# Kernel optimization log

Measured on AMD Instinct MI355X. Metric: run time of the kernel, lower is better.

## Reference

```python
import jax, jax.numpy as jnp
import numpy as np


def _adj(p):
    # p: [B,N,C] -> W = exp(-pairwise squared distance), fully dense (incl. self loops)
    sq = jnp.sum(p * p, axis=-1, keepdims=True)            # [B,N,1]
    d = sq - 2.0 * jnp.einsum('bnc,bmc->bnm', p, p) + jnp.swapaxes(sq, 1, 2)
    return jnp.exp(-d)


def _cheb_lap(W):
    # PyG ChebConv norm with sym normalization, lambda_max=2: L_hat = L - I = -D^{-1/2} W D^{-1/2}
    dinv = jax.lax.rsqrt(jnp.sum(W, axis=-1))              # [B,N]
    return -(dinv[:, :, None] * W * dinv[:, None, :])


def _reg_lap(W):
    # get_laplacian(sym) after remove_self_loops: L = I - D'^{-1/2} W' D'^{-1/2}, W' = W with zero diag
    N = W.shape[1]
    eye = jnp.eye(N, dtype=W.dtype)
    W0 = W * (1.0 - eye)
    dinv = jax.lax.rsqrt(jnp.sum(W0, axis=-1))
    return eye - dinv[:, :, None] * W0 * dinv[:, None, :]


def _cheb(x, Lhat, Wk, b):
    # Chebyshev recursion: Z0=x, Z1=L_hat x, Zk = 2 L_hat Z_{k-1} - Z_{k-2}
    # x: [B,N,Cin], Lhat: [B,N,N], Wk: [K,Cin,Cout]
    Z0 = x
    out = jnp.einsum('bni,io->bno', Z0, Wk[0])
    if Wk.shape[0] > 1:
        Z1 = jnp.einsum('bnm,bmi->bni', Lhat, x)
        out = out + jnp.einsum('bni,io->bno', Z1, Wk[1])
        for k in range(2, Wk.shape[0]):
            Z2 = 2.0 * jnp.einsum('bnm,bmi->bni', Lhat, Z1) - Z0
            out = out + jnp.einsum('bni,io->bno', Z2, Wk[k])
            Z0, Z1 = Z1, Z2
    return out + b


def _reg(out, L):
    # ||out^T L out||_F, block-diagonal L -> sum over batch blocks
    M = jnp.einsum('bnc,bnm,bmd->cd', out, L, out)
    return jnp.linalg.norm(M)


def setup_inputs() -> dict:
    key = jax.random.key(0)
    ks = jax.random.split(key, 16)
    B, N = 16, 1024
    s = 0.05
    return {
        'x': jax.random.normal(ks[0], (B, N, 6), dtype=jnp.float32),
        'batch': jnp.repeat(jnp.arange(B, dtype=jnp.int64 if jax.config.jax_enable_x64 else jnp.int32), N),
        'batch_size': B,
        'nr_points': N,
        'w1': jax.random.normal(ks[1], (6, 6, 128), dtype=jnp.float32) * s,
        'b1': jnp.zeros((128,), dtype=jnp.float32),
        'w2': jax.random.normal(ks[2], (5, 128, 512), dtype=jnp.float32) * s,
        'b2': jnp.zeros((512,), dtype=jnp.float32),
        'w3': jax.random.normal(ks[3], (3, 512, 1024), dtype=jnp.float32) * s,
        'b3': jnp.zeros((1024,), dtype=jnp.float32),
        'fw1': jax.random.normal(ks[4], (1024, 512), dtype=jnp.float32) * s,
        'fb1': jnp.zeros((512,), dtype=jnp.float32),
        'fw2': jax.random.normal(ks[5], (512, 128), dtype=jnp.float32) * s,
        'fb2': jnp.zeros((128,), dtype=jnp.float32),
        'fw3': jax.random.normal(ks[6], (128, 10), dtype=jnp.float32) * s,
        'fb3': jnp.zeros((10,), dtype=jnp.float32),
    }


def reference(x, batch, batch_size, nr_points, w1, b1, w2, b2, w3, b3,
              fw1, fb1, fw2, fb2, fw3, fb3):
    sg = jax.lax.stop_gradient
    # reshape of x happens inside torch.no_grad -> input to conv1 is detached
    h = sg(x)
    W1 = sg(_adj(x))
    out = jax.nn.relu(_cheb(h, _cheb_lap(W1), w1, b1))            # [B,N,128]
    r1 = sg(_reg(out, _reg_lap(W1)))
    W2 = sg(_adj(out))
    out = jax.nn.relu(_cheb(out, sg(_cheb_lap(W2)), w2, b2))      # [B,N,512]
    r2 = sg(_reg(out, _reg_lap(W2)))
    W3 = sg(_adj(out))
    out = jax.nn.relu(_cheb(out, sg(_cheb_lap(W3)), w3, b3))      # [B,N,1024]
    r3 = sg(_reg(out, _reg_lap(W3)))
    pooled = jnp.max(out, axis=1)                                  # MaxPool1d over points
    h = jax.nn.relu(pooled @ fw1 + fb1)
    h = jax.nn.relu(h @ fw2 + fb2)
    logits = h @ fw3 + fb3
    return logits, r1, r2, r3
```

## Files before the change

kernel.cpp:

```cpp
#include <hip/hip_runtime.h>

#define BB 16
#define NN 1024
#define LDT 16384

typedef float4 f4;
typedef __attribute__((ext_vector_type(8))) short bf16x8;
typedef __attribute__((ext_vector_type(4))) float f32x4;

__device__ __forceinline__ unsigned f2b1(float f) {
    unsigned u = __builtin_bit_cast(unsigned, f);
    return (u + 0x7fffu + ((u >> 16) & 1u)) >> 16;
}
__device__ __forceinline__ float b2f1(unsigned s) {
    unsigned u = (s & 0xffffu) << 16;
    return __builtin_bit_cast(float, u);
}

#define SW(r, k) ((r) * 64 + ((k) ^ (((((r) & 7) ^ (((r) >> 3) & 7))) << 3)))

__device__ __forceinline__ void gload16(const unsigned short* g, short* l) {
    __builtin_amdgcn_global_load_lds(
        (const __attribute__((address_space(1))) unsigned int*)g,
        (__attribute__((address_space(3))) unsigned int*)l, 16, 0, 0);
}

__device__ __forceinline__ float wave_sum(float v) {
    #pragma unroll
    for (int m = 32; m >= 1; m >>= 1) v += __shfl_xor(v, m);
    return v;
}
__device__ __forceinline__ float wave_max(float v) {
    #pragma unroll
    for (int m = 32; m >= 1; m >>= 1) v = fmaxf(v, __shfl_xor(v, m));
    return v;
}

__device__ __forceinline__ void stage_tr(short* T, const unsigned short* src,
                                         size_t col_base, int c0, int Cvalid, int tid) {
    #pragma unroll
    for (int n = 0; n < 2; n++) {
        int q = n * 256 + tid;
        int p = q >> 4, h = q & 15;
        int cg = c0 + 2 * p;
        uint4 r0 = make_uint4(0, 0, 0, 0), r1 = make_uint4(0, 0, 0, 0);
        if (cg < Cvalid)     r0 = *(const uint4*)&src[(size_t)cg * LDT + col_base + 8 * h];
        if (cg + 1 < Cvalid) r1 = *(const uint4*)&src[(size_t)(cg + 1) * LDT + col_base + 8 * h];
        const unsigned* a0 = (const unsigned*)&r0;
        const unsigned* a1 = (const unsigned*)&r1;
        #pragma unroll
        for (int e = 0; e < 8; e++) {
            unsigned lo = (e & 1) ? (a0[e >> 1] >> 16) : (a0[e >> 1] & 0xffffu);
            unsigned hi = (e & 1) ? (a1[e >> 1] >> 16) : (a1[e >> 1] & 0xffffu);
            int r = 8 * h + e;
            *(unsigned*)&T[SW(r, 2 * p)] = lo | (hi << 16);
        }
    }
}

__global__ void xt_prep_kernel(const float* __restrict__ x, short* __restrict__ xh,
                               short* __restrict__ xl) {
    int m = blockIdx.x * 256 + threadIdx.x;
    #pragma unroll
    for (int c = 0; c < 8; c++) {
        float v = (c < 6) ? x[(size_t)m * 6 + c] : 0.f;
        unsigned h = f2b1(v);
        unsigned l = f2b1(v - b2f1(h));
        xh[(size_t)c * LDT + m] = (short)h;
        xl[(size_t)c * LDT + m] = (short)l;
    }
}

__global__ void wtt_prep_kernel(const float* __restrict__ Wk, short* __restrict__ WtT,
                                int Kp64, int KpValid, int CpadM1, int shift, int Cin, int Cout) {
    int idx = blockIdx.x * 256 + threadIdx.x;
    if (idx >= Cout * Kp64) return;
    int co = idx / Kp64, kk = idx - co * Kp64;
    int c = kk & CpadM1;
    float val = 0.f;
    if (kk < KpValid && c < Cin)
        val = Wk[((size_t)(kk >> shift) * Cin + c) * Cout + co];
    WtT[(size_t)co * Kp64 + kk] = (short)f2b1(val);
}

__global__ void wtrans_kernel(const float* __restrict__ Wt, float* __restrict__ WtT,
                              int K, int O) {
    int idx = blockIdx.x * 256 + threadIdx.x;
    if (idx >= K * O) return;
    int o = idx / K, k = idx - o * K;
    WtT[idx] = Wt[(size_t)k * O + o];
}

__global__ void scale_sc_kernel(const short* __restrict__ src, const float* __restrict__ coeff,
                                short* __restrict__ dst, int total8) {
    int q = blockIdx.x * 256 + threadIdx.x;
    if (q >= total8) return;
    size_t base = (size_t)q * 8;
    int m8 = (int)(base & (LDT - 1));
    uint4 v = *(const uint4*)&((const unsigned short*)src)[base];
    f4 c0 = *(const f4*)&coeff[m8];
    f4 c1 = *(const f4*)&coeff[m8 + 4];
    const float* cp0 = (const float*)&c0;
    const float* cp1 = (const float*)&c1;
    unsigned* vp = (unsigned*)&v;
    #pragma unroll
    for (int e = 0; e < 4; e++) {
        float se0 = (e < 2) ? cp0[2 * e] : cp1[2 * e - 4];
        float se1 = (e < 2) ? cp0[2 * e + 1] : cp1[2 * e - 3];
        vp[e] = f2b1(b2f1(vp[e]) * se0) | (f2b1(b2f1(vp[e] >> 16) * se1) << 16);
    }
    *(uint4*)&((unsigned short*)dst)[base] = v;
}

__global__ __launch_bounds__(256)
void xpose_kernel(const short* __restrict__ H, const short* __restrict__ L,
                  int Cvalid, int CR, short* __restrict__ XRh, short* __restrict__ XRl) {
    __shared__ short Th[128 * 64], Tl[128 * 64];
    int tid = threadIdx.x;
    int m0 = blockIdx.x * 128, c0 = blockIdx.y * 64;
    stage_tr(Th, (const unsigned short*)H, m0, c0, Cvalid, tid);
    stage_tr(Tl, (const unsigned short*)L, m0, c0, Cvalid, tid);
    __syncthreads();
    #pragma unroll
    for (int n = 0; n < 4; n++) {
        int q = n * 256 + tid;
        int r = q >> 3, j = q & 7;
        int g = (r & 7) ^ ((r >> 3) & 7);
        *(uint4*)&XRh[(size_t)(m0 + r) * CR + c0 + 8 * j] = *(const uint4*)&Th[r * 64 + 8 * (j ^ g)];
        *(uint4*)&XRl[(size_t)(m0 + r) * CR + c0 + 8 * j] = *(const uint4*)&Tl[r * 64 + 8 * (j ^ g)];
    }
}

__global__ void sqt_part_kernel(const short* __restrict__ H, const short* __restrict__ L,
                                int C, float* __restrict__ dst) {
    int m = blockIdx.x * 256 + threadIdx.x;
    int cb = blockIdx.y * 128;
    int ce = min(cb + 128, C);
    const unsigned short* Hp = (const unsigned short*)H;
    const unsigned short* Lp = (const unsigned short*)L;
    float s = 0.f;
    for (int c = cb; c < ce; c++) {
        float v = b2f1(Hp[(size_t)c * LDT + m]) + b2f1(Lp[(size_t)c * LDT + m]);
        s += v * v;
    }
    dst[(size_t)blockIdx.y * LDT + m] = s;
}
__global__ void sqt_red_kernel(const float* __restrict__ part, int NC, float* __restrict__ sq) {
    int m = blockIdx.x * 256 + threadIdx.x;
    float s = 0.f;
    for (int y = 0; y < NC; y++) s += part[(size_t)y * LDT + m];
    sq[m] = s;
}

__global__ __launch_bounds__(256)
void adj_mfma_kernel(const short* __restrict__ XRh, const short* __restrict__ XRl,
                     int ck64, int CR, const float* __restrict__ sq,
                     short* __restrict__ Wb, float* __restrict__ Wpart,
                     float* __restrict__ diagW) {
    __shared__ short Ah[128 * 64], Al[128 * 64], Bh[128 * 64], Bl[128 * 64];
    __shared__ float jpart[128][2];
    int tid = threadIdx.x, lane = tid & 63, w = tid >> 6;
    int wj = w >> 1, wi = w & 1;
    int b = blockIdx.z, i0 = blockIdx.x * 128, j0 = blockIdx.y * 128;
    size_t bo = (size_t)b * NN;
    f32x4 acc[4][4] = {};
    const unsigned short* Hp = (const unsigned short*)XRh;
    const unsigned short* Lp = (const unsigned short*)XRl;
    int rr = lane >> 3, jj = lane & 7;
    size_t offI[4], offJ[4];
    #pragma unroll
    for (int m = 0; m < 4; m++) {
        int s = w + m * 4;
        int jc = jj ^ rr ^ (s & 7);
        offI[m] = (size_t)(bo + i0 + 8 * s + rr) * CR + 8 * jc;
        offJ[m] = (size_t)(bo + j0 + 8 * s + rr) * CR + 8 * jc;
    }
    for (int t = 0; t < ck64; t++) {
        int c0 = t * 64;
        #pragma unroll
        for (int m = 0; m < 4; m++) {
            int s512 = (w + m * 4) * 512;
            gload16(Hp + offI[m] + c0, Ah + s512);
            gload16(Lp + offI[m] + c0, Al + s512);
            gload16(Hp + offJ[m] + c0, Bh + s512);
            gload16(Lp + offJ[m] + c0, Bl + s512);
        }
        __syncthreads();
        int la = lane & 15;
        #pragma unroll
        for (int ks = 0; ks < 2; ks++) {
            int kb = ks * 32 + (lane >> 4) * 8;
            bf16x8 jh[4], jl[4], ih[4], il[4];
            #pragma unroll
            for (int f = 0; f < 4; f++) {
                int jr = wj * 64 + f * 16 + la;
                jh[f] = *(const bf16x8*)&Bh[SW(jr, kb)];
                jl[f] = *(const bf16x8*)&Bl[SW(jr, kb)];
                int ir = wi * 64 + f * 16 + la;
                ih[f] = *(const bf16x8*)&Ah[SW(ir, kb)];
                il[f] = *(const bf16x8*)&Al[SW(ir, kb)];
            }
            #pragma unroll
            for (int fq = 0; fq < 4; fq++)
                #pragma unroll
                for (int fi = 0; fi < 4; fi++) {
                    acc[fq][fi] = __builtin_amdgcn_mfma_f32_16x16x32_bf16(jh[fq], ih[fi], acc[fq][fi], 0, 0, 0);
                    acc[fq][fi] = __builtin_amdgcn_mfma_f32_16x16x32_bf16(jh[fq], il[fi], acc[fq][fi], 0, 0, 0);
                    acc[fq][fi] = __builtin_amdgcn_mfma_f32_16x16x32_bf16(jl[fq], ih[fi], acc[fq][fi], 0, 0, 0);
                }
        }
        __syncthreads();
    }
    const float* sqb = sq + bo;
    unsigned short* Wout = (unsigned short*)Wb + bo * NN;
    float si_[4];
    int iloc[4];
    #pragma unroll
    for (int fi = 0; fi < 4; fi++) {
        iloc[fi] = i0 + wi * 64 + fi * 16 + (lane & 15);
        si_[fi] = sqb[iloc[fi]];
    }
    #pragma unroll
    for (int fq = 0; fq < 4; fq++) {
        int jb = j0 + wj * 64 + fq * 16 + (lane >> 4) * 4;
        #pragma unroll
        for (int r = 0; r < 4; r++) {
            int j = jb + r;
            float sj = sqb[j];
            float p = 0.f;
            #pragma unroll
            for (int fi = 0; fi < 4; fi++) {
                float val = __expf(2.f * ((const float*)&acc[fq][fi])[r] - si_[fi] - sj);
                Wout[(size_t)j * NN + iloc[fi]] = (unsigned short)f2b1(val);
                if (iloc[fi] == j) diagW[bo + j] = val;
                else p += val;
            }
            p += __shfl_xor(p, 1); p += __shfl_xor(p, 2);
            p += __shfl_xor(p, 4); p += __shfl_xor(p, 8);
            if ((lane & 15) == 0)
                jpart[wj * 64 + fq * 16 + (lane >> 4) * 4 + r][wi] = p;
        }
    }
    __syncthreads();
    if (tid < 128)
        Wpart[(size_t)blockIdx.x * (BB * NN) + bo + j0 + tid] = jpart[tid][0] + jpart[tid][1];
}

__global__ void reduce_prep_kernel(const float* __restrict__ Wpart, const float* __restrict__ diagW,
                                   float* dinv, float* dinvP, float* cA1, float* cA2, float* cAV) {
    int idx = blockIdx.x * 256 + threadIdx.x;
    float s = 0.f;
    #pragma unroll
    for (int x = 0; x < 8; x++) s += Wpart[(size_t)x * (BB * NN) + idx];
    float d = diagW[idx];
    float dv = rsqrtf(s + d);
    float dp = rsqrtf(s);
    dinv[idx] = dv; dinvP[idx] = dp;
    cA1[idx] = -dv; cA2[idx] = -2.f * dv; cAV[idx] = -dp;
}

template<bool HAS_PREV, bool SKIP_DIAG, bool WRITE_SC, int XB>
__global__ __launch_bounds__(512)
void wgemm2_kernel(const short* __restrict__ W, const short* __restrict__ Bsc,
                   const float* __restrict__ cAvec, float prevSign,
                   const short* __restrict__ PrevT, const float* __restrict__ scVec,
                   short* __restrict__ DstT, short* __restrict__ DstSc, int Cvalid) {
    __shared__ short As[2][XB * 64], Bs[2][128 * 64];
    constexpr int NFI = XB / 64;
    int tid = threadIdx.x, lane = tid & 63, w = tid >> 6;
    int wcc = w >> 2, wii = w & 3;
    int b = blockIdx.z, i0 = blockIdx.x * XB, c0 = blockIdx.y * 128;
    size_t bo = (size_t)b * NN;
    const unsigned short* Wp = (const unsigned short*)W + bo * NN;
    const unsigned short* Bp = (const unsigned short*)Bsc;
    int rr = lane >> 3, jj = lane & 7;
    int jc = jj ^ rr ^ (w & 7);
    const unsigned short* aR0 = Wp + (size_t)(i0 + 8 * w + rr) * NN + 8 * jc;
    const unsigned short* aR1 = Wp + (size_t)(i0 + 8 * ((XB == 128) ? w + 8 : w) + rr) * NN + 8 * jc;
    const unsigned short* bR0 = Bp + (size_t)(c0 + 8 * w + rr) * LDT + bo + 8 * jc;
    const unsigned short* bR1 = Bp + (size_t)(c0 + 8 * (w + 8) + rr) * LDT + bo + 8 * jc;
    int aO0 = w * 512;
    int aO1 = ((XB == 128) ? w + 8 : w) * 512;
    int bO0 = w * 512, bO1 = (w + 8) * 512;
    auto STAGE = [&](int k0, int buf) {
        gload16(aR0 + k0, As[buf] + aO0);
        if (XB == 128) gload16(aR1 + k0, As[buf] + aO1);
        gload16(bR0 + k0, Bs[buf] + bO0);
        gload16(bR1 + k0, Bs[buf] + bO1);
    };
    f32x4 acc[4][NFI] = {};
    STAGE(0, 0);
    __syncthreads();
    int cur = 0;
    for (int t = 0; t < NN / 64; t++) {
        int k0 = t * 64;
        bool more = (t + 1 < NN / 64);
        if (more) STAGE(k0 + 64, cur ^ 1);
        if (SKIP_DIAG) {
            if (k0 >= i0 && k0 < i0 + XB) {
                if (tid < 64) As[cur][SW((k0 - i0) + tid, tid)] = 0;
                __syncthreads();
            }
        }
        int la = lane & 15;
        #pragma unroll
        for (int ks = 0; ks < 2; ks++) {
            int kb = ks * 32 + (lane >> 4) * 8;
            bf16x8 ac[4], bi[NFI];
            #pragma unroll
            for (int f = 0; f < 4; f++) ac[f] = *(const bf16x8*)&Bs[cur][SW(wcc * 64 + f * 16 + la, kb)];
            #pragma unroll
            for (int f = 0; f < NFI; f++) bi[f] = *(const bf16x8*)&As[cur][SW(wii * (XB / 4) + f * 16 + la, kb)];
            #pragma unroll
            for (int fq = 0; fq < 4; fq++)
                #pragma unroll
                for (int fi = 0; fi < NFI; fi++)
                    acc[fq][fi] = __builtin_amdgcn_mfma_f32_16x16x32_bf16(ac[fq], bi[fi], acc[fq][fi], 0, 0, 0);
        }
        if (more) __syncthreads();
        cur ^= 1;
    }
    const unsigned short* Pp = (const unsigned short*)PrevT;
    unsigned short* Dp = (unsigned short*)DstT;
    unsigned short* Sp = (unsigned short*)DstSc;
    #pragma unroll
    for (int fi = 0; fi < NFI; fi++) {
        int i = i0 + wii * (XB / 4) + fi * 16 + (lane & 15);
        float ca = cAvec[bo + i];
        float sc = WRITE_SC ? scVec[bo + i] : 0.f;
        #pragma unroll
        for (int fq = 0; fq < 4; fq++) {
            int cb = c0 + wcc * 64 + fq * 16 + (lane >> 4) * 4;
            const float* av = (const float*)&acc[fq][fi];
            #pragma unroll
            for (int r = 0; r < 4; r++) {
                int c = cb + r;
                if (c < Cvalid) {
                    float v = ca * av[r];
                    if (HAS_PREV) v += prevSign * b2f1(Pp[(size_t)c * LDT + bo + i]);
                    Dp[(size_t)c * LDT + bo + i] = (unsigned short)f2b1(v);
                    if (WRITE_SC) Sp[(size_t)c * LDT + bo + i] = (unsigned short)f2b1(v * sc);
                }
            }
        }
    }
}

__global__ __launch_bounds__(512)
void fgemm_mfma_kernel(const short* __restrict__ A0T, const short* __restrict__ ZrT,
                       const short* __restrict__ WtT, int Kp64, int KpValid, int Cpad,
                       const float* __restrict__ bias,
                       short* __restrict__ OutH, short* __restrict__ OutL) {
    __shared__ short As[2][128 * 64], Bs[2][128 * 64];
    int tid = threadIdx.x, lane = tid & 63, w = tid >> 6;
    int wco = w >> 2, wm = w & 3;
    int m0 = blockIdx.x * 128, co0 = blockIdx.y * 128;
    const unsigned short* A0 = (const unsigned short*)A0T;
    const unsigned short* Zr = (const unsigned short*)ZrT;
    const unsigned short* Wt = (const unsigned short*)WtT;
    int rr = lane >> 3, jj = lane & 7;
    int jcB = jj ^ rr ^ (w & 7);
    const unsigned short* bB0 = Wt + (size_t)(co0 + 8 * w + rr) * Kp64 + 8 * jcB;
    const unsigned short* bB1 = Wt + (size_t)(co0 + 8 * (w + 8) + rr) * Kp64 + 8 * jcB;
    int bO0 = w * 512, bO1 = (w + 8) * 512;
    int p = tid >> 4, h = tid & 15;
    uint4 ra0, ra1;
    auto loadA = [&](int kk0) {
        int kg0 = kk0 + 2 * p;
        ra0 = make_uint4(0, 0, 0, 0); ra1 = make_uint4(0, 0, 0, 0);
        if (kg0 < KpValid) {
            const unsigned short* s0 = (kg0 < Cpad) ? (A0 + (size_t)kg0 * LDT)
                                                    : (Zr + (size_t)(kg0 - Cpad) * LDT);
            ra0 = *(const uint4*)&s0[m0 + 8 * h];
        }
        if (kg0 + 1 < KpValid) {
            int kg1 = kg0 + 1;
            const unsigned short* s1 = (kg1 < Cpad) ? (A0 + (size_t)kg1 * LDT)
                                                    : (Zr + (size_t)(kg1 - Cpad) * LDT);
            ra1 = *(const uint4*)&s1[m0 + 8 * h];
        }
    };
    auto unpackA = [&](int buf) {
        const unsigned* a0 = (const unsigned*)&ra0;
        const unsigned* a1 = (const unsigned*)&ra1;
        #pragma unroll
        for (int e = 0; e < 8; e++) {
            unsigned lo = (e & 1) ? (a0[e >> 1] >> 16) : (a0[e >> 1] & 0xffffu);
            unsigned hi = (e & 1) ? (a1[e >> 1] >> 16) : (a1[e >> 1] & 0xffffu);
            *(unsigned*)&As[buf][SW(8 * h + e, 2 * p)] = lo | (hi << 16);
        }
    };
    f32x4 acc[4][2] = {};
    loadA(0);
    gload16(bB0, Bs[0] + bO0);
    gload16(bB1, Bs[0] + bO1);
    unpackA(0);
    __syncthreads();
    int cur = 0;
    for (int kk0 = 0; kk0 < Kp64; kk0 += 64) {
        bool more = (kk0 + 64 < Kp64);
        if (more) {
            loadA(kk0 + 64);
            gload16(bB0 + kk0 + 64, Bs[cur ^ 1] + bO0);
            gload16(bB1 + kk0 + 64, Bs[cur ^ 1] + bO1);
        }
        int la = lane & 15;
        #pragma unroll
        for (int ks = 0; ks < 2; ks++) {
            int kb = ks * 32 + (lane >> 4) * 8;
            bf16x8 ac[4], bm[2];
            #pragma unroll
            for (int f = 0; f < 4; f++) ac[f] = *(const bf16x8*)&Bs[cur][SW(wco * 64 + f * 16 + la, kb)];
            #pragma unroll
            for (int f = 0; f < 2; f++) bm[f] = *(const bf16x8*)&As[cur][SW(wm * 32 + f * 16 + la, kb)];
            #pragma unroll
            for (int fq = 0; fq < 4; fq++)
                #pragma unroll
                for (int fi = 0; fi < 2; fi++)
                    acc[fq][fi] = __builtin_amdgcn_mfma_f32_16x16x32_bf16(ac[fq], bm[fi], acc[fq][fi], 0, 0, 0);
        }
        if (more) {
            unpackA(cur ^ 1);
            __syncthreads();
        }
        cur ^= 1;
    }
    unsigned short* OH = (unsigned short*)OutH;
    unsigned short* OL = (unsigned short*)OutL;
    #pragma unroll
    for (int fi = 0; fi < 2; fi++) {
        int m = m0 + wm * 32 + fi * 16 + (lane & 15);
        #pragma unroll
        for (int fq = 0; fq < 4; fq++) {
            int cb = co0 + wco * 64 + fq * 16 + (lane >> 4) * 4;
            const float* av = (const float*)&acc[fq][fi];
            #pragma unroll
            for (int r = 0; r < 4; r++) {
                int co = cb + r;
                float v = av[r] + bias[co];
                v = v > 0.f ? v : 0.f;
                unsigned ph = f2b1(v);
                unsigned pl = f2b1(v - b2f1(ph));
                OH[(size_t)co * LDT + m] = (unsigned short)ph;
                OL[(size_t)co * LDT + m] = (unsigned short)pl;
            }
        }
    }
}

__global__ __launch_bounds__(256)
void mgemm_mfma_kernel(const short* __restrict__ XT, const short* __restrict__ VT,
                       float* __restrict__ Mpart, int Cout, int kChunk) {
    __shared__ short As[128 * 64], Bs[128 * 64];
    int tid = threadIdx.x, lane = tid & 63, w = tid >> 6;
    int wcj = w >> 1, wci = w & 1;
    int ci0 = blockIdx.x * 128, cj0 = blockIdx.y * 128;
    int kStart = blockIdx.z * kChunk;
    const unsigned short* Xp = (const unsigned short*)XT + (size_t)ci0 * LDT;
    const unsigned short* Vp = (const unsigned short*)VT + (size_t)cj0 * LDT;
    int rr = lane >> 3, jj = lane & 7;
    const unsigned short* aB[4];
    const unsigned short* bB[4];
    short* aL[4]; short* bL[4];
    #pragma unroll
    for (int n = 0; n < 4; n++) {
        int s = w + n * 4;
        int jc = jj ^ rr ^ (s & 7);
        aB[n] = Xp + (size_t)(8 * s + rr) * LDT + 8 * jc;
        bB[n] = Vp + (size_t)(8 * s + rr) * LDT + 8 * jc;
        aL[n] = As + s * 512; bL[n] = Bs + s * 512;
    }
    f32x4 acc[4][4] = {};
    for (int k0 = kStart; k0 < kStart + kChunk; k0 += 64) {
        #pragma unroll
        for (int n = 0; n < 4; n++) {
            gload16(aB[n] + k0, aL[n]);
            gload16(bB[n] + k0, bL[n]);
        }
        __syncthreads();
        int la = lane & 15;
        #pragma unroll
        for (int ks = 0; ks < 2; ks++) {
            int kb = ks * 32 + (lane >> 4) * 8;
            bf16x8 aj[4], bi[4];
            #pragma unroll
            for (int f = 0; f < 4; f++) {
                aj[f] = *(const bf16x8*)&Bs[SW(wcj * 64 + f * 16 + la, kb)];
                bi[f] = *(const bf16x8*)&As[SW(wci * 64 + f * 16 + la, kb)];
            }
            #pragma unroll
            for (int fq = 0; fq < 4; fq++)
                #pragma unroll
                for (int fi = 0; fi < 4; fi++)
                    acc[fq][fi] = __builtin_amdgcn_mfma_f32_16x16x32_bf16(aj[fq], bi[fi], acc[fq][fi], 0, 0, 0);
        }
        __syncthreads();
    }
    float* pt = Mpart + (size_t)blockIdx.z * Cout * Cout;
    #pragma unroll
    for (int fq = 0; fq < 4; fq++) {
        int cjb = cj0 + wcj * 64 + fq * 16 + (lane >> 4) * 4;
        #pragma unroll
        for (int fi = 0; fi < 4; fi++) {
            int ci = ci0 + wci * 64 + fi * 16 + (lane & 15);
            const float* av = (const float*)&acc[fq][fi];
            #pragma unroll
            for (int r = 0; r < 4; r++)
                pt[(size_t)(cjb + r) * Cout + ci] = av[r];
        }
    }
}

__global__ void fro1_kernel(const float* __restrict__ part, int nElem, int splitk,
                            float* __restrict__ blockSS) {
    int tid = threadIdx.x;
    float ss = 0.f;
    for (int idx = blockIdx.x * 256 + tid; idx < nElem; idx += 1024 * 256) {
        float s = 0.f;
        for (int z = 0; z < splitk; z++) s += part[(size_t)z * nElem + idx];
        ss += s * s;
    }
    __shared__ float red[256];
    red[tid] = ss; __syncthreads();
    for (int m = 128; m >= 1; m >>= 1) { if (tid < m) red[tid] += red[tid + m]; __syncthreads(); }
    if (tid == 0) blockSS[blockIdx.x] = red[0];
}
__global__ void fro2_kernel(const float* __restrict__ blockSS, float* __restrict__ outp) {
    int tid = threadIdx.x;
    float s = 0.f;
    for (int i = tid; i < 1024; i += 256) s += blockSS[i];
    __shared__ float red[256];
    red[tid] = s; __syncthreads();
    for (int m = 128; m >= 1; m >>= 1) { if (tid < m) red[tid] += red[tid + m]; __syncthreads(); }
    if (tid == 0) *outp = sqrtf(red[0]);
}

__global__ void pool_kernel(const short* __restrict__ H, const short* __restrict__ L,
                            float* __restrict__ out) {
    int wave = threadIdx.x >> 6, lane = threadIdx.x & 63;
    int r = blockIdx.x * 4 + wave;
    int co = r >> 4, b = r & 15;
    const unsigned short* h = (const unsigned short*)H + (size_t)co * LDT + b * NN;
    const unsigned short* l = (const unsigned short*)L + (size_t)co * LDT + b * NN;
    float m = -1e30f;
    #pragma unroll
    for (int it = 0; it < 2; it++) {
        int n8 = (it * 64 + lane) * 8;
        uint4 vh = *(const uint4*)&h[n8];
        uint4 vl = *(const uint4*)&l[n8];
        const unsigned* hp = (const unsigned*)&vh;
        const unsigned* lp = (const unsigned*)&vl;
        #pragma unroll
        for (int e = 0; e < 4; e++) {
            m = fmaxf(m, b2f1(hp[e]) + b2f1(lp[e]));
            m = fmaxf(m, b2f1(hp[e] >> 16) + b2f1(lp[e] >> 16));
        }
    }
    m = wave_max(m);
    if (lane == 0) out[b * 1024 + co] = m;
}

__global__ void fc_kernel(const float* __restrict__ in, const float* __restrict__ WtT,
                          const float* __restrict__ bias, float* __restrict__ out,
                          int K, int O, int doRelu) {
    int wave = threadIdx.x >> 6, lane = threadIdx.x & 63;
    int idx = blockIdx.x * 4 + wave;
    if (idx >= 16 * O) return;
    int b = idx / O, o = idx - b * O;
    const float* ib = in + (size_t)b * K;
    const float* wr = WtT + (size_t)o * K;
    float s = 0.f;
    for (int k = lane * 4; k < K; k += 256) {
        f4 a = *(const f4*)&ib[k];
        f4 wv = *(const f4*)&wr[k];
        s += a.x * wv.x + a.y * wv.y + a.z * wv.z + a.w * wv.w;
    }
    s = wave_sum(s);
    if (lane == 0) {
        s += bias[o];
        if (doRelu) s = fmaxf(s, 0.f);
        out[(size_t)b * O + o] = s;
    }
}

extern "C" void kernel_launch(void* const* d_in, const int* in_sizes, int n_in,
                              void* d_out, int out_size, void* d_ws, size_t ws_size,
                              hipStream_t stream) {
    const float* x   = (const float*)d_in[0];
    const float* w1  = (const float*)d_in[4];
    const float* b1  = (const float*)d_in[5];
    const float* w2  = (const float*)d_in[6];
    const float* b2  = (const float*)d_in[7];
    const float* w3  = (const float*)d_in[8];
    const float* b3  = (const float*)d_in[9];
    const float* fw1 = (const float*)d_in[10];
    const float* fb1 = (const float*)d_in[11];
    const float* fw2 = (const float*)d_in[12];
    const float* fb2 = (const float*)d_in[13];
    const float* fw3 = (const float*)d_in[14];
    const float* fb3 = (const float*)d_in[15];
    float* out = (float*)d_out;

    char* ws = (char*)d_ws;
    size_t off = 0;
    auto alloc = [&](size_t bytes) -> void* {
        void* p = ws + off; off += (bytes + 255) & ~(size_t)255; return p;
    };
    short* Wbuf = (short*)alloc((size_t)BB * NN * NN * 2);
    short* Zbuf = (short*)alloc((size_t)1024 * LDT * 2);
    short* ZSc  = (short*)alloc((size_t)1024 * LDT * 2);
    short* Z0Sc = (short*)alloc((size_t)512 * LDT * 2);
    short* XRh  = (short*)alloc((size_t)512 * LDT * 2);
    short* XRl  = (short*)alloc((size_t)512 * LDT * 2);
    short* o1H  = (short*)alloc((size_t)128 * LDT * 2);
    short* o1L  = (short*)alloc((size_t)128 * LDT * 2);
    short* o2H  = (short*)alloc((size_t)512 * LDT * 2);
    short* o2L  = (short*)alloc((size_t)512 * LDT * 2);
    short* o3H  = (short*)alloc((size_t)1024 * LDT * 2);
    short* o3L  = (short*)alloc((size_t)1024 * LDT * 2);
    short* xTh  = (short*)alloc((size_t)8 * LDT * 2);
    short* xTl  = (short*)alloc((size_t)8 * LDT * 2);
    short* WtT  = (short*)alloc((size_t)1024 * 1536 * 2);
    float* fwT1 = (float*)alloc((size_t)512 * 1024 * 4);
    float* fwT2 = (float*)alloc((size_t)128 * 512 * 4);
    float* fwT3 = (float*)alloc((size_t)10 * 128 * 4);
    float* sqpart = (float*)alloc((size_t)8 * LDT * 4);
    float* Wpart  = (float*)alloc((size_t)8 * BB * NN * 4);
    float* diagW  = (float*)alloc(BB * NN * 4);
    float* sq    = (float*)alloc(BB * NN * 4);
    float* dinv  = (float*)alloc(BB * NN * 4);
    float* dinvP = (float*)alloc(BB * NN * 4);
    float* cA1   = (float*)alloc(BB * NN * 4);
    float* cA2   = (float*)alloc(BB * NN * 4);
    float* cAV   = (float*)alloc(BB * NN * 4);
    float* pooled= (float*)alloc(BB * 1024 * 4);
    float* h1    = (float*)alloc(BB * 512 * 4);
    float* h2    = (float*)alloc(BB * 128 * 4);
    float* blockSS = (float*)alloc(1024 * 4);
    float* Mpart = (float*)Wbuf;
    (void)ws_size; (void)in_sizes; (void)n_in; (void)out_size;

    struct Layer {
        const short *XTh, *XTl;
        int C, K, Cpad, shift, Kp64, KpValid, Cout, splitk, rIdx;
        const float *Wk, *bk;
        short *OutH, *OutL;
    };
    Layer L[3] = {
        { xTh, xTl, 8,   6, 8,   3, 64,   48,   128,  64, 160, w1, b1, o1H, o1L },
        { o1H, o1L, 128, 5, 128, 7, 640,  640,  512,  32, 161, w2, b2, o2H, o2L },
        { o2H, o2L, 512, 3, 512, 9, 1536, 1536, 1024, 8,  162, w3, b3, o3H, o3L },
    };

    xt_prep_kernel<<<LDT / 256, 256, 0, stream>>>(x, xTh, xTl);
    wtrans_kernel<<<(1024 * 512 + 255) / 256, 256, 0, stream>>>(fw1, fwT1, 1024, 512);
    wtrans_kernel<<<(512 * 128 + 255) / 256, 256, 0, stream>>>(fw2, fwT2, 512, 128);
    wtrans_kernel<<<(128 * 10 + 255) / 256, 256, 0, stream>>>(fw3, fwT3, 128, 10);

    for (int l = 0; l < 3; l++) {
        const Layer& P = L[l];
        int NC = (P.C + 127) / 128;
        int CR = (P.Cpad < 64) ? 64 : P.Cpad;
        wtt_prep_kernel<<<(P.Cout * P.Kp64 + 255) / 256, 256, 0, stream>>>(
            P.Wk, WtT, P.Kp64, P.KpValid, P.Cpad - 1, P.shift, (l == 0) ? 6 : P.C, P.Cout);
        sqt_part_kernel<<<dim3(LDT / 256, NC), 256, 0, stream>>>(P.XTh, P.XTl, P.C, sqpart);
        sqt_red_kernel<<<LDT / 256, 256, 0, stream>>>(sqpart, NC, sq);
        xpose_kernel<<<dim3(LDT / 128, CR / 64), 256, 0, stream>>>(
            P.XTh, P.XTl, P.Cpad, CR, XRh, XRl);
        adj_mfma_kernel<<<dim3(8, 8, BB), 256, 0, stream>>>(XRh, XRl, CR / 64, CR, sq,
                                                            Wbuf, Wpart, diagW);
        reduce_prep_kernel<<<BB * NN / 256, 256, 0, stream>>>(Wpart, diagW, dinv, dinvP, cA1, cA2, cAV);

        scale_sc_kernel<<<(P.Cpad * LDT / 8 + 255) / 256, 256, 0, stream>>>(
            P.XTh, dinv, Z0Sc, P.Cpad * LDT / 8);

        int cT = (P.Cpad + 127) / 128;
        bool sm = (P.Cpad <= 128);
        auto sliceR = [&](int k) -> short* { return Zbuf + (size_t)(k - 1) * P.Cpad * LDT; };
        auto sliceS = [&](int k) -> short* { return ZSc  + (size_t)(k - 1) * P.Cpad * LDT; };
        if (P.K > 2) {
            if (sm) wgemm2_kernel<false, false, true, 64><<<dim3(NN / 64, cT, BB), 512, 0, stream>>>(
                        Wbuf, Z0Sc, cA1, 0.f, (const short*)nullptr, dinv, sliceR(1), sliceS(1), P.Cpad);
            else    wgemm2_kernel<false, false, true, 128><<<dim3(NN / 128, cT, BB), 512, 0, stream>>>(
                        Wbuf, Z0Sc, cA1, 0.f, (const short*)nullptr, dinv, sliceR(1), sliceS(1), P.Cpad);
        } else {
            if (sm) wgemm2_kernel<false, false, false, 64><<<dim3(NN / 64, cT, BB), 512, 0, stream>>>(
                        Wbuf, Z0Sc, cA1, 0.f, (const short*)nullptr, dinv, sliceR(1), (short*)nullptr, P.Cpad);
            else    wgemm2_kernel<false, false, false, 128><<<dim3(NN / 128, cT, BB), 512, 0, stream>>>(
                        Wbuf, Z0Sc, cA1, 0.f, (const short*)nullptr, dinv, sliceR(1), (short*)nullptr, P.Cpad);
        }
        for (int k = 2; k < P.K; k++) {
            const short* prevT = (k == 2) ? P.XTh : sliceR(k - 2);
            if (k < P.K - 1) {
                if (sm) wgemm2_kernel<true, false, true, 64><<<dim3(NN / 64, cT, BB), 512, 0, stream>>>(
                            Wbuf, sliceS(k - 1), cA2, -1.f, prevT, dinv, sliceR(k), sliceS(k), P.Cpad);
                else    wgemm2_kernel<true, false, true, 128><<<dim3(NN / 128, cT, BB), 512, 0, stream>>>(
                            Wbuf, sliceS(k - 1), cA2, -1.f, prevT, dinv, sliceR(k), sliceS(k), P.Cpad);
            } else {
                if (sm) wgemm2_kernel<true, false, false, 64><<<dim3(NN / 64, cT, BB), 512, 0, stream>>>(
                            Wbuf, sliceS(k - 1), cA2, -1.f, prevT, dinv, sliceR(k), (short*)nullptr, P.Cpad);
                else    wgemm2_kernel<true, false, false, 128><<<dim3(NN / 128, cT, BB), 512, 0, stream>>>(
                            Wbuf, sliceS(k - 1), cA2, -1.f, prevT, dinv, sliceR(k), (short*)nullptr, P.Cpad);
            }
        }
        fgemm_mfma_kernel<<<dim3(LDT / 128, P.Cout / 128), 512, 0, stream>>>(
            P.XTh, Zbuf, WtT, P.Kp64, P.KpValid, P.Cpad, P.bk, P.OutH, P.OutL);
        scale_sc_kernel<<<(P.Cout * LDT / 8 + 255) / 256, 256, 0, stream>>>(
            P.OutH, dinvP, ZSc, P.Cout * LDT / 8);
        int cTV = P.Cout / 128;
        if (P.Cout <= 128)
            wgemm2_kernel<true, true, false, 64><<<dim3(NN / 64, cTV, BB), 512, 0, stream>>>(
                Wbuf, ZSc, cAV, 1.f, P.OutH, dinvP, Zbuf, (short*)nullptr, P.Cout);
        else
            wgemm2_kernel<true, true, false, 128><<<dim3(NN / 128, cTV, BB), 512, 0, stream>>>(
                Wbuf, ZSc, cAV, 1.f, P.OutH, dinvP, Zbuf, (short*)nullptr, P.Cout);
        int kChunk = LDT / P.splitk;
        mgemm_mfma_kernel<<<dim3(P.Cout / 128, P.Cout / 128, P.splitk), 256, 0, stream>>>(
            P.OutH, Zbuf, Mpart, P.Cout, kChunk);
        fro1_kernel<<<1024, 256, 0, stream>>>(Mpart, P.Cout * P.Cout, P.splitk, blockSS);
        fro2_kernel<<<1, 256, 0, stream>>>(blockSS, out + P.rIdx);
    }
    pool_kernel<<<16384 / 4, 256, 0, stream>>>(o3H, o3L, pooled);
    fc_kernel<<<(16 * 512 + 3) / 4, 256, 0, stream>>>(pooled, fwT1, fb1, h1, 1024, 512, 1);
    fc_kernel<<<(16 * 128 + 3) / 4, 256, 0, stream>>>(h1, fwT2, fb2, h2, 512, 128, 1);
    fc_kernel<<<(16 * 10 + 3) / 4, 256, 0, stream>>>(h2, fwT3, fb3, out, 128, 10, 0);
}
```

Measured before the change: 897.1 us.

## Fuse squared-norm partials into transpose kernel and double-buffer mgemm LDS tiles

Removes the separate sqt_part kernel by computing per-point squared norms from the shared-memory tiles already staged in xpose_kernel, so the strided reads of H and L over all channels happen only once. The reduction now runs over CR/64 partial chunks instead of C/128. Separately, mgemm_mfma_kernel gets two LDS buffers so the global-to-LDS load of the next k-tile overlaps the MFMA work on the current one, at the cost of doubled shared memory and possibly lower occupancy. Correctness relies on the staged tile zero-filling channels beyond Cvalid.

```diff
diff --git a/kernel.cpp b/kernel.cpp
--- a/kernel.cpp
+++ b/kernel.cpp
@@ -114,7 +114,8 @@
 
 __global__ __launch_bounds__(256)
 void xpose_kernel(const short* __restrict__ H, const short* __restrict__ L,
-                  int Cvalid, int CR, short* __restrict__ XRh, short* __restrict__ XRl) {
+                  int Cvalid, int CR, short* __restrict__ XRh, short* __restrict__ XRl,
+                  float* __restrict__ sqpart) {
     __shared__ short Th[128 * 64], Tl[128 * 64];
     int tid = threadIdx.x;
     int m0 = blockIdx.x * 128, c0 = blockIdx.y * 64;
@@ -129,22 +130,22 @@
         *(uint4*)&XRh[(size_t)(m0 + r) * CR + c0 + 8 * j] = *(const uint4*)&Th[r * 64 + 8 * (j ^ g)];
         *(uint4*)&XRl[(size_t)(m0 + r) * CR + c0 + 8 * j] = *(const uint4*)&Tl[r * 64 + 8 * (j ^ g)];
     }
-}
-
-__global__ void sqt_part_kernel(const short* __restrict__ H, const short* __restrict__ L,
-                                int C, float* __restrict__ dst) {
-    int m = blockIdx.x * 256 + threadIdx.x;
-    int cb = blockIdx.y * 128;
-    int ce = min(cb + 128, C);
-    const unsigned short* Hp = (const unsigned short*)H;
-    const unsigned short* Lp = (const unsigned short*)L;
-    float s = 0.f;
-    for (int c = cb; c < ce; c++) {
-        float v = b2f1(Hp[(size_t)c * LDT + m]) + b2f1(Lp[(size_t)c * LDT + m]);
-        s += v * v;
-    }
-    dst[(size_t)blockIdx.y * LDT + m] = s;
-}
+    {
+        int r = tid >> 1, half = tid & 1;
+        const unsigned short* Thp = (const unsigned short*)Th;
+        const unsigned short* Tlp = (const unsigned short*)Tl;
+        float s = 0.f;
+        #pragma unroll
+        for (int k = 0; k < 32; k++) {
+            int kk = half * 32 + k;
+            float v = b2f1(Thp[SW(r, kk)]) + b2f1(Tlp[SW(r, kk)]);
+            s += v * v;
+        }
+        s += __shfl_xor(s, 1);
+        if (half == 0) sqpart[(size_t)blockIdx.y * LDT + m0 + r] = s;
+    }
+}
+
 __global__ void sqt_red_kernel(const float* __restrict__ part, int NC, float* __restrict__ sq) {
     int m = blockIdx.x * 256 + threadIdx.x;
     float s = 0.f;
@@ -451,7 +452,7 @@
 __global__ __launch_bounds__(256)
 void mgemm_mfma_kernel(const short* __restrict__ XT, const short* __restrict__ VT,
                        float* __restrict__ Mpart, int Cout, int kChunk) {
-    __shared__ short As[128 * 64], Bs[128 * 64];
+    __shared__ short As[2][128 * 64], Bs[2][128 * 64];
     int tid = threadIdx.x, lane = tid & 63, w = tid >> 6;
     int wcj = w >> 1, wci = w & 1;
     int ci0 = blockIdx.x * 128, cj0 = blockIdx.y * 128;
@@ -461,23 +462,31 @@
     int rr = lane >> 3, jj = lane & 7;
     const unsigned short* aB[4];
     const unsigned short* bB[4];
-    short* aL[4]; short* bL[4];
+    int sO[4];
     #pragma unroll
     for (int n = 0; n < 4; n++) {
         int s = w + n * 4;
         int jc = jj ^ rr ^ (s & 7);
         aB[n] = Xp + (size_t)(8 * s + rr) * LDT + 8 * jc;
         bB[n] = Vp + (size_t)(8 * s + rr) * LDT + 8 * jc;
-        aL[n] = As + s * 512; bL[n] = Bs + s * 512;
-    }
+        sO[n] = s * 512;
+    }
+    auto STAGE = [&](int k0, int buf) {
+        #pragma unroll
+        for (int n = 0; n < 4; n++) {
+            gload16(aB[n] + k0, As[buf] + sO[n]);
+            gload16(bB[n] + k0, Bs[buf] + sO[n]);
+        }
+    };
     f32x4 acc[4][4] = {};
-    for (int k0 = kStart; k0 < kStart + kChunk; k0 += 64) {
-        #pragma unroll
-        for (int n = 0; n < 4; n++) {
-            gload16(aB[n] + k0, aL[n]);
-            gload16(bB[n] + k0, bL[n]);
-        }
-        __syncthreads();
+    STAGE(kStart, 0);
+    __syncthreads();
+    int cur = 0;
+    int nt = kChunk / 64;
+    for (int t = 0; t < nt; t++) {
+        int k0 = kStart + t * 64;
+        bool more = (t + 1 < nt);
+        if (more) STAGE(k0 + 64, cur ^ 1);
         int la = lane & 15;
         #pragma unroll
         for (int ks = 0; ks < 2; ks++) {
@@ -485,8 +494,8 @@
             bf16x8 aj[4], bi[4];
             #pragma unroll
             for (int f = 0; f < 4; f++) {
-                aj[f] = *(const bf16x8*)&Bs[SW(wcj * 64 + f * 16 + la, kb)];
-                bi[f] = *(const bf16x8*)&As[SW(wci * 64 + f * 16 + la, kb)];
+                aj[f] = *(const bf16x8*)&Bs[cur][SW(wcj * 64 + f * 16 + la, kb)];
+                bi[f] = *(const bf16x8*)&As[cur][SW(wci * 64 + f * 16 + la, kb)];
             }
             #pragma unroll
             for (int fq = 0; fq < 4; fq++)
@@ -494,7 +503,8 @@
                 for (int fi = 0; fi < 4; fi++)
                     acc[fq][fi] = __builtin_amdgcn_mfma_f32_16x16x32_bf16(aj[fq], bi[fi], acc[fq][fi], 0, 0, 0);
         }
-        __syncthreads();
+        if (more) __syncthreads();
+        cur ^= 1;
     }
     float* pt = Mpart + (size_t)blockIdx.z * Cout * Cout;
     #pragma unroll
@@ -659,14 +669,12 @@
 
     for (int l = 0; l < 3; l++) {
         const Layer& P = L[l];
-        int NC = (P.C + 127) / 128;
         int CR = (P.Cpad < 64) ? 64 : P.Cpad;
         wtt_prep_kernel<<<(P.Cout * P.Kp64 + 255) / 256, 256, 0, stream>>>(
             P.Wk, WtT, P.Kp64, P.KpValid, P.Cpad - 1, P.shift, (l == 0) ? 6 : P.C, P.Cout);
-        sqt_part_kernel<<<dim3(LDT / 256, NC), 256, 0, stream>>>(P.XTh, P.XTl, P.C, sqpart);
-        sqt_red_kernel<<<LDT / 256, 256, 0, stream>>>(sqpart, NC, sq);
         xpose_kernel<<<dim3(LDT / 128, CR / 64), 256, 0, stream>>>(
-            P.XTh, P.XTl, P.Cpad, CR, XRh, XRl);
+            P.XTh, P.XTl, P.Cpad, CR, XRh, XRl, sqpart);
+        sqt_red_kernel<<<LDT / 256, 256, 0, stream>>>(sqpart, CR / 64, sq);
         adj_mfma_kernel<<<dim3(8, 8, BB), 256, 0, stream>>>(XRh, XRl, CR / 64, CR, sq,
                                                             Wbuf, Wpart, diagW);
         reduce_prep_kernel<<<BB * NN / 256, 256, 0, stream>>>(Wpart, diagW, dinv, dinvP, cA1, cA2, cAV);
```

Measured after the change: 820.4 us (median of 2 runs). 1.09x faster.
